# Optimization experiments

Hardware: AMD Instinct MI355X
Metric: run time of the kernel (lower is better)

## Reference

```python
import jax, jax.numpy as jnp
import numpy as np

SCALE = 16.0
IGNORE_THRES = 0.5
NUM_CLASSES = 40
ANCHORS_PX = np.array([[16., 16.], [32., 32.], [64., 64.], [32., 64.], [64., 32.]], dtype=np.float32)
NB, NA, NH, NW, MAXT = 16, 5, 96, 96, 50


def setup_inputs() -> dict:
    key = jax.random.key(0)
    k1, k2, k3, k4, k5, k6, k7 = jax.random.split(key, 7)
    prediction = jax.random.normal(k1, (NB, NA, NH, NW, 5 + NUM_CLASSES), jnp.float32)
    # GT boxes in pixel space; x in [0, NW*SCALE), y in [0, NH*SCALE)
    xs = jax.random.uniform(k2, (NB, MAXT), minval=0.5, maxval=NW - 0.5) * SCALE
    ys = jax.random.uniform(k3, (NB, MAXT), minval=0.5, maxval=NH - 0.5) * SCALE
    hs = jax.random.uniform(k4, (NB, MAXT), minval=0.5, maxval=6.0) * SCALE
    ws = jax.random.uniform(k5, (NB, MAXT), minval=0.5, maxval=6.0) * SCALE
    lbl = jax.random.randint(k6, (NB, MAXT), 0, NUM_CLASSES)
    target = jnp.zeros((NB, MAXT, 13 + NUM_CLASSES), jnp.float32)
    target = target.at[..., 0].set(xs).at[..., 1].set(ys)
    target = target.at[..., 3].set(hs).at[..., 4].set(ws)  # source reads h from col 3, w from col 4
    target = target.at[..., 13:].set(jax.nn.one_hot(lbl, NUM_CLASSES, dtype=jnp.float32))
    target_sizes = jax.random.randint(k7, (NB,), 20, MAXT + 1)
    return {"prediction": prediction, "target": target, "target_sizes": target_sizes}


def _iou_xywh(g, p):
    # center/size boxes -> corners, with the original's +1 pixel convention
    g_x1, g_x2 = g[0] - g[2] / 2, g[0] + g[2] / 2
    g_y1, g_y2 = g[1] - g[3] / 2, g[1] + g[3] / 2
    p_x1, p_x2 = p[0] - p[2] / 2, p[0] + p[2] / 2
    p_y1, p_y2 = p[1] - p[3] / 2, p[1] + p[3] / 2
    iw = jnp.clip(jnp.minimum(g_x2, p_x2) - jnp.maximum(g_x1, p_x1) + 1., 0.)
    ih = jnp.clip(jnp.minimum(g_y2, p_y2) - jnp.maximum(g_y1, p_y1) + 1., 0.)
    inter = iw * ih
    ga = (g_x2 - g_x1 + 1.) * (g_y2 - g_y1 + 1.)
    pa = (p_x2 - p_x1 + 1.) * (p_y2 - p_y1 + 1.)
    return inter / (ga + pa - inter + 1e-16)


def _build_targets(pred_boxes, pred_conf, pred_cls, target, target_sizes, anchors):
    # Sequential scan over (batch, gt) preserves the torch double-loop's
    nB, nA, nH, nW = pred_conf.shape
    maxT = target.shape[1]
    aw, ah = anchors[:, 0], anchors[:, 1]
    anch_area = (aw + 1.) * (ah + 1.)
    mask = jnp.zeros((nB, nA, nH, nW), jnp.float32)
    conf_mask = jnp.ones((nB, nA, nH, nW), jnp.float32)
    tx = jnp.zeros_like(mask); ty = jnp.zeros_like(mask)
    tw = jnp.zeros_like(mask); th = jnp.zeros_like(mask)
    tconf = jnp.zeros_like(mask)
    tlabel = jnp.zeros((nB, nA, nH, nW), jnp.int32)  # argmax of one-hot tcls

    def step(carry, bt):
        mask, conf_mask, tx, ty, tw, th, tconf, tlabel, nGT, nCorrect = carry
        b = bt // maxT
        t = bt % maxT
        valid = t < target_sizes[b]
        row = target[b, t]
        gx = row[0] / SCALE; gy = row[1] / SCALE
        gw = row[4] / SCALE; gh = row[3] / SCALE  # w from col 4, h from col 3 (as in source)
        gi = gx.astype(jnp.int32); gj = gy.astype(jnp.int32)
        # anchor IoU: both boxes anchored at origin, corner-style with +1 (x1y1x2y2=True path)
        inter = jnp.clip(jnp.minimum(gw, aw) + 1., 0.) * jnp.clip(jnp.minimum(gh, ah) + 1., 0.)
        anch_ious = inter / ((gw + 1.) * (gh + 1.) + anch_area - inter + 1e-16)
        bd = jnp.where(valid, b, nB)  # out-of-bounds batch index -> scatter dropped when padded
        cur = conf_mask[b, :, gj, gi]
        conf_mask = conf_mask.at[bd, :, gj, gi].set(jnp.where(anch_ious > IGNORE_THRES, 0., cur), mode='drop')
        best_n = jnp.argmax(anch_ious)
        mask = mask.at[bd, best_n, gj, gi].set(1., mode='drop')
        conf_mask = conf_mask.at[bd, best_n, gj, gi].set(1., mode='drop')
        tx = tx.at[bd, best_n, gj, gi].set(gx - gi.astype(jnp.float32), mode='drop')
        ty = ty.at[bd, best_n, gj, gi].set(gy - gj.astype(jnp.float32), mode='drop')
        tw = tw.at[bd, best_n, gj, gi].set(jnp.log(gw / aw[best_n] + 1e-16), mode='drop')
        th = th.at[bd, best_n, gj, gi].set(jnp.log(gh / ah[best_n] + 1e-16), mode='drop')
        lbl = jnp.argmax(row[13:]).astype(jnp.int32)
        tlabel = tlabel.at[bd, best_n, gj, gi].set(lbl, mode='drop')
        tconf = tconf.at[bd, best_n, gj, gi].set(1., mode='drop')
        iou = _iou_xywh(jnp.stack([gx, gy, gw, gh]), pred_boxes[b, best_n, gj, gi])
        correct = valid & (iou > 0.5) & (jnp.argmax(pred_cls[b, best_n, gj, gi]) == lbl) & (pred_conf[b, best_n, gj, gi] > 0.5)
        return (mask, conf_mask, tx, ty, tw, th, tconf, tlabel,
                nGT + valid.astype(jnp.int32), nCorrect + correct.astype(jnp.int32)), None

    init = (mask, conf_mask, tx, ty, tw, th, tconf, tlabel,
            jnp.array(0, jnp.int32), jnp.array(0, jnp.int32))
    (mask, conf_mask, tx, ty, tw, th, tconf, tlabel, nGT, nCorrect), _ = jax.lax.scan(
        step, init, jnp.arange(nB * maxT))
    return mask, conf_mask, tx, ty, tw, th, tconf, tlabel, nGT, nCorrect


def _yolo_loss(prediction, target, target_sizes):
    nB, nA, nH, nW = prediction.shape[:4]
    pred_conf = prediction[..., 0]
    x = prediction[..., 1]; y = prediction[..., 2]
    h = prediction[..., 3]; w = prediction[..., 4]
    pred_cls = prediction[..., 5:]
    grid_x = jnp.arange(nW, dtype=jnp.float32).reshape(1, 1, 1, nW)
    grid_y = jnp.arange(nH, dtype=jnp.float32).reshape(1, 1, nH, 1)
    anchors = jnp.asarray(ANCHORS_PX) / SCALE  # grid units
    aw = anchors[:, 0].reshape(1, nA, 1, 1)
    ah = anchors[:, 1].reshape(1, nA, 1, 1)
    pred_boxes = jnp.stack([
        x + grid_x, y + grid_y, jnp.exp(w) * aw * jnp.ones_like(w), jnp.exp(h) * ah * jnp.ones_like(h)
    ], axis=-1)
    sg = jax.lax.stop_gradient  # torch uses .cpu().data inside build_targets
    mask, conf_mask, tx, ty, tw, th, tconf, tlabel, nGT, nCorrect = _build_targets(
        sg(pred_boxes), sg(pred_conf), sg(pred_cls), target, target_sizes, anchors)
    nM = jnp.sum(mask)
    mmean = lambda v: jnp.sum(mask * v) / nM  # masked MSE mean (size_average=True)
    loss_x = mmean((x - tx) ** 2)
    loss_y = mmean((y - ty) ** 2)
    loss_w = mmean((w - tw) ** 2)
    loss_h = mmean((h - th) ** 2)
    # BCEWithLogits, numerically stable
    bce = jnp.maximum(pred_conf, 0.) - pred_conf * tconf + jnp.log1p(jnp.exp(-jnp.abs(pred_conf)))
    # torch: conf_mask_false = (conf_mask - mask) as byte used as boolean mask -> nonzero selects
    cmf = (conf_mask != mask).astype(jnp.float32)
    loss_conf = jnp.sum(cmf * bce) / jnp.sum(cmf) + jnp.sum(mask * bce) / nM
    logp = jax.nn.log_softmax(pred_cls, axis=-1)
    ce = -jnp.take_along_axis(logp, tlabel[..., None], axis=-1)[..., 0]
    loss_cls = (1.0 / nB) * jnp.sum(mask * ce) / nM
    loss = loss_x + loss_y + loss_w + loss_h + loss_conf + loss_cls
    nProposals = jnp.sum(pred_conf > 0).astype(jnp.float32)
    recall = nCorrect.astype(jnp.float32) / jnp.maximum(nGT, 1).astype(jnp.float32)
    precision = jnp.where(nProposals > 0, nCorrect.astype(jnp.float32) / jnp.maximum(nProposals, 1.), 1.0)
    return (loss, loss_x + loss_y + loss_w + loss_h, loss_conf, loss_cls, recall, precision)


def reference(prediction, target, target_sizes):
    return _yolo_loss(prediction, target, target_sizes)
```

## Files before the change

kernel.cpp:

```cpp
#include <hip/hip_runtime.h>
#include <math.h>

#define NB 16
#define NA 5
#define NH 96
#define NW 96
#define MAXT 50
#define NC 40
#define CH 45
#define TGT_W 53
#define NCELL (NH*NW)
#define NTGT (NB*MAXT)
#define TOTF4 8294400
#define CONF_BLOCKS 2025
#define CONF_STRIDE 2073600
#define IGNORE_THRES 0.5f

__device__ __constant__ float c_AW[5] = {1.f, 2.f, 4.f, 2.f, 4.f};
__device__ __constant__ float c_AH[5] = {1.f, 2.f, 4.f, 4.f, 2.f};


__device__ __forceinline__ float softplusf(float p) {
    return fmaxf(p, 0.f) + log1pf(expf(-fabsf(p)));
}

__device__ __forceinline__ float pick(float4 q, int comp) {
    return comp == 0 ? q.x : comp == 1 ? q.y : comp == 2 ? q.z : q.w;
}

__global__ __launch_bounds__(64) void tgt_phase1(
    const float* __restrict__ pred, const float* __restrict__ tgt,
    const int* __restrict__ tsz, double* acc, int* iacc,
    int* keyG, int* metaG, float* fxG, float* fyG, float* gwG, float* ghG) {
    const int bt = blockIdx.x;
    const int b = bt / MAXT, t = bt % MAXT;
    const int lane = threadIdx.x;

    if (bt == 0) {
        if (lane < 10) acc[lane] = 0.0;
        if (lane < 2)  iacc[lane] = 0;
    }

    const bool valid = t < tsz[b];
    const float* row = tgt + (size_t)bt * TGT_W;
    const float inv_s = 0.0625f;
    float gx = row[0] * inv_s, gy = row[1] * inv_s;
    float gh_ = row[3] * inv_s, gw_ = row[4] * inv_s;
    int gi = (int)gx, gj = (int)gy;

    float lv = (lane < NC) ? row[13 + lane] : -1e30f;
    int   li = (lane < NC) ? lane : (1 << 30);
    #pragma unroll
    for (int off = 32; off; off >>= 1) {
        float ov = __shfl_xor(lv, off);
        int   oi = __shfl_xor(li, off);
        if (ov > lv || (ov == lv && oi < li)) { lv = ov; li = oi; }
    }
    int lbl = li;

    float best_iou = -1e30f; int best = 0; int ign = 0;
    #pragma unroll
    for (int a = 0; a < 5; ++a) {
        float iw = fmaxf(fminf(gw_, c_AW[a]) + 1.f, 0.f);
        float ih = fmaxf(fminf(gh_, c_AH[a]) + 1.f, 0.f);
        float inter = iw * ih;
        float iou = inter / ((gw_ + 1.f) * (gh_ + 1.f) +
                             (c_AW[a] + 1.f) * (c_AH[a] + 1.f) - inter + 1e-16f);
        if (iou > IGNORE_THRES) ign |= (1 << a);
        if (iou > best_iou) { best_iou = iou; best = a; }
    }

    size_t pbase = ((((size_t)b * NA + best) * NH + gj) * NW + gi) * CH;
    float pv = (lane < CH) ? pred[pbase + lane] : -1e30f;
    float pc = __shfl(pv, 0);
    float px = __shfl(pv, 1) + (float)gi;
    float py = __shfl(pv, 2) + (float)gj;
    float ph = expf(__shfl(pv, 3)) * c_AH[best];
    float pw = expf(__shfl(pv, 4)) * c_AW[best];

    float gx1 = gx - gw_ * 0.5f, gx2 = gx + gw_ * 0.5f;
    float gy1 = gy - gh_ * 0.5f, gy2 = gy + gh_ * 0.5f;
    float px1 = px - pw * 0.5f, px2 = px + pw * 0.5f;
    float py1 = py - ph * 0.5f, py2 = py + ph * 0.5f;
    float iw2 = fmaxf(fminf(gx2, px2) - fmaxf(gx1, px1) + 1.f, 0.f);
    float ih2 = fmaxf(fminf(gy2, py2) - fmaxf(gy1, py1) + 1.f, 0.f);
    float inter2 = iw2 * ih2;
    float ga = (gx2 - gx1 + 1.f) * (gy2 - gy1 + 1.f);
    float pa = (px2 - px1 + 1.f) * (py2 - py1 + 1.f);
    float iou2 = inter2 / (ga + pa - inter2 + 1e-16f);

    float cv = (lane >= 5 && lane < CH) ? pv : -1e30f;
    int   ci = (lane >= 5 && lane < CH) ? (lane - 5) : (1 << 30);
    #pragma unroll
    for (int off = 32; off; off >>= 1) {
        float ov = __shfl_xor(cv, off);
        int   oi = __shfl_xor(ci, off);
        if (ov > cv || (ov == cv && oi < ci)) { cv = ov; ci = oi; }
    }
    bool correct = valid && (iou2 > 0.5f) && (ci == lbl) && (pc > 0.5f);

    if (lane == 0) {
        keyG[bt]  = valid ? (gj * NW + gi) : -1;
        metaG[bt] = best | (ign << 3) | (lbl << 8) | ((correct ? 1 : 0) << 14);
        fxG[bt] = gx - (float)gi; fyG[bt] = gy - (float)gj;
        gwG[bt] = gw_;            ghG[bt] = gh_;
    }
}

__global__ __launch_bounds__(64) void ownership(
    const int* __restrict__ keyG, const int* __restrict__ metaG,
    int* iacc, int* wlist) {
    __shared__ int sk[MAXT], sm[MAXT];
    const int b = blockIdx.x, t = threadIdx.x;
    if (t < MAXT) { sk[t] = keyG[b * MAXT + t]; sm[t] = metaG[b * MAXT + t]; }
    __syncthreads();
    if (t >= MAXT) return;
    const int myKey = sk[t];
    if (myKey < 0) return;
    for (int u = t + 1; u < MAXT; ++u)
        if (sk[u] == myKey) return;

    int cm = 0x1F, m = 0;
    int w[5] = {-1, -1, -1, -1, -1};
    for (int u = 0; u < MAXT; ++u) {
        if (sk[u] != myKey) continue;
        int mu = sm[u];
        cm &= ~((mu >> 3) & 0x1F);
        int bn = mu & 7;
        cm |= (1 << bn); m |= (1 << bn);
        w[bn] = u;
    }
    int pos = atomicAdd(&iacc[1], 5);
    #pragma unroll
    for (int a = 0; a < 5; ++a) {
        int ca = (b * NA + a) * NCELL + myKey;
        int flags = ca | (((m >> a) & 1) << 20) | (((cm >> a) & 1) << 21);
        wlist[2 * (pos + a)]     = flags;
        wlist[2 * (pos + a) + 1] = ((m >> a) & 1) ? (b * MAXT + w[a]) : -1;
    }
}

__global__ __launch_bounds__(1024) void corrections(
    const float* __restrict__ pred, double* acc, const int* __restrict__ iacc,
    const int* __restrict__ wlist, const int* __restrict__ metaG,
    const float* __restrict__ fxG, const float* __restrict__ fyG,
    const float* __restrict__ gwG, const float* __restrict__ ghG) {
    const int wave = threadIdx.x >> 6, lane = threadIdx.x & 63;
    const int idx = blockIdx.x * 16 + wave;
    const int count = iacc[1];
    double loc[9];
    #pragma unroll
    for (int c = 0; c < 9; ++c) loc[c] = 0.0;

    if (idx < count) {
        int flags = wlist[2 * idx], writer = wlist[2 * idx + 1];
        int ca = flags & 0xFFFFF;
        int ma = (flags >> 20) & 1, cma = (flags >> 21) & 1;
        size_t base = (size_t)ca * CH;
        float v = (lane < CH) ? pred[base + lane] : -1e30f;
        float p = __shfl(v, 0);
        float s0 = softplusf(p);
        int cmf = (cma != ma) ? 1 : 0;
        loc[0] = (cmf ? (double)(s0 - p * (float)ma) : 0.0) - (double)s0;
        loc[1] = (double)(cmf - 1);
        if (ma) {
            loc[2] = (double)(s0 - p);
            loc[8] = 1.0;
            float x = __shfl(v, 1), y = __shfl(v, 2);
            float hh = __shfl(v, 3), wv = __shfl(v, 4);
            float fx = fxG[writer], fy = fyG[writer];
            float gww = gwG[writer], ghh = ghG[writer];
            int a = (ca / NCELL) % NA;
            int lbl = (metaG[writer] >> 8) & 0x3F;
            float tw_ = logf(gww / c_AW[a] + 1e-16f);
            float th_ = logf(ghh / c_AH[a] + 1e-16f);
            loc[4] = (double)((x - fx) * (x - fx));
            loc[5] = (double)((y - fy) * (y - fy));
            loc[6] = (double)((wv - tw_) * (wv - tw_));
            loc[7] = (double)((hh - th_) * (hh - th_));
            float cvv = (lane >= 5 && lane < CH) ? v : -1e30f;
            float mx = cvv;
            #pragma unroll
            for (int off = 32; off; off >>= 1) mx = fmaxf(mx, __shfl_xor(mx, off));
            float e = (lane >= 5 && lane < CH) ? expf(v - mx) : 0.f;
            #pragma unroll
            for (int off = 32; off; off >>= 1) e += __shfl_xor(e, off);
            float cll = __shfl(v, 5 + lbl);
            loc[3] = (double)(logf(e) + mx - cll);
        }
    }

    __shared__ double red[16][9];
    if (lane == 0) {
        #pragma unroll
        for (int c = 0; c < 9; ++c) red[wave][c] = loc[c];
    }
    __syncthreads();
    if (threadIdx.x < 9) {
        double s = 0.0;
        #pragma unroll
        for (int wv = 0; wv < 16; ++wv) s += red[wv][threadIdx.x];
        if (s != 0.0) atomicAdd(&acc[1 + threadIdx.x], s);
    }
}

__global__ __launch_bounds__(1024) void conf_pass3(
    const float4* __restrict__ pf, double* partial_d, int* partial_i) {
    const int tid = blockIdx.x * 1024 + threadIdx.x;
    float4 q0 = pf[tid];
    float4 q1 = pf[tid + CONF_STRIDE];
    float4 q2 = pf[tid + 2 * CONF_STRIDE];
    float4 q3 = pf[tid + 3 * CONF_STRIDE];

    float bce = 0.f; int prop = 0;
    int r = tid % 45;
    if (r == 0 || r == 11 || r == 22 || r == 33) {
        int comp = r / 11;
        float c0 = pick(q0, comp), c1 = pick(q1, comp);
        float c2 = pick(q2, comp), c3 = pick(q3, comp);
        bce = softplusf(c0) + softplusf(c1) + softplusf(c2) + softplusf(c3);
        prop = (c0 > 0.f) + (c1 > 0.f) + (c2 > 0.f) + (c3 > 0.f);
    }

    #pragma unroll
    for (int off = 32; off; off >>= 1) {
        bce  += __shfl_down(bce, off);
        prop += __shfl_down(prop, off);
    }
    __shared__ float sb[16];
    __shared__ int   sp[16];
    int wid = threadIdx.x >> 6, lane = threadIdx.x & 63;
    if (lane == 0) { sb[wid] = bce; sp[wid] = prop; }
    __syncthreads();
    if (threadIdx.x == 0) {
        float tb = 0.f; int tp = 0;
        #pragma unroll
        for (int w = 0; w < 16; ++w) { tb += sb[w]; tp += sp[w]; }
        partial_d[blockIdx.x] = (double)tb;
        partial_i[blockIdx.x] = tp;
    }
}

__global__ __launch_bounds__(256) void finalize(
    const double* __restrict__ acc, const int* __restrict__ iacc,
    const int* __restrict__ tsz, const int* __restrict__ metaG,
    const double* __restrict__ partial_d, const int* __restrict__ partial_i,
    float* out) {
    __shared__ double sd[256];
    __shared__ int    si[256], sc[256];
    double db = 0.0; int ip = 0, cor = 0;
    for (int i = threadIdx.x; i < CONF_BLOCKS; i += 256) { db += partial_d[i]; ip += partial_i[i]; }
    for (int i = threadIdx.x; i < NTGT; i += 256) cor += (metaG[i] >> 14) & 1;
    sd[threadIdx.x] = db; si[threadIdx.x] = ip; sc[threadIdx.x] = cor;
    __syncthreads();
    for (int off = 128; off; off >>= 1) {
        if (threadIdx.x < off) {
            sd[threadIdx.x] += sd[threadIdx.x + off];
            si[threadIdx.x] += si[threadIdx.x + off];
            sc[threadIdx.x] += sc[threadIdx.x + off];
        }
        __syncthreads();
    }
    if (threadIdx.x != 0) return;
    double sum_bce0 = sd[0];
    int nProp = si[0], nCor = sc[0];
    int nGT = 0;
    for (int b = 0; b < NB; ++b) nGT += tsz[b];

    double nM = acc[9];
    double inv_nM = 1.0 / (nM > 0.0 ? nM : 1e-16);
    double l_coord = (acc[5] + acc[6] + acc[7] + acc[8]) * inv_nM;
    double sum_cmf = (double)(NB * NA * NH * NW) + acc[2];
    double l_conf = (sum_bce0 + acc[1]) / sum_cmf + acc[3] * inv_nM;
    double l_cls = (1.0 / (double)NB) * acc[4] * inv_nM;
    double loss = l_coord + l_conf + l_cls;
    float recall = (float)nCor / (float)(nGT > 1 ? nGT : 1);
    float precision = (nProp > 0) ? ((float)nCor / fmaxf((float)nProp, 1.f)) : 1.f;
    out[0] = (float)loss;
    out[1] = (float)l_coord;
    out[2] = (float)l_conf;
    out[3] = (float)l_cls;
    out[4] = recall;
    out[5] = precision;
}

extern "C" void kernel_launch(void* const* d_in, const int* in_sizes, int n_in,
                              void* d_out, int out_size, void* d_ws, size_t ws_size,
                              hipStream_t stream) {
    const float* pred = (const float*)d_in[0];
    const float* tgt  = (const float*)d_in[1];
    const int*   tsz  = (const int*)d_in[2];
    float* out = (float*)d_out;

    double* acc = (double*)d_ws;
    int* iacc   = (int*)((char*)d_ws + 80);
    int* keyG   = (int*)((char*)d_ws + 96);
    int* metaG  = keyG + NTGT;
    float* fxG  = (float*)(metaG + NTGT);
    float* fyG  = fxG + NTGT;
    float* gwG  = fyG + NTGT;
    float* ghG  = gwG + NTGT;
    int* wlist  = (int*)(ghG + NTGT);
    double* partial_d = (double*)((char*)d_ws + 51296);
    int*    partial_i = (int*)((char*)d_ws + 67496);

    tgt_phase1<<<NTGT, 64, 0, stream>>>(pred, tgt, tsz, acc, iacc,
                                        keyG, metaG, fxG, fyG, gwG, ghG);
    ownership<<<NB, 64, 0, stream>>>(keyG, metaG, iacc, wlist);
    corrections<<<250, 1024, 0, stream>>>(pred, acc, iacc, wlist,
                                          metaG, fxG, fyG, gwG, ghG);
    conf_pass3<<<CONF_BLOCKS, 1024, 0, stream>>>((const float4*)pred, partial_d, partial_i);
    finalize<<<1, 256, 0, stream>>>(acc, iacc, tsz, metaG, partial_d, partial_i, out);
}
```

Baseline: 217.9 us.

## Fuse target building with ownership and merge corrections into the conf pass

Merges the per-target and ownership kernels into a single per-batch kernel that uses shared memory. It writes fixed slots containing precomputed targets, which removes the atomic slot counter. The corrections pass and the full confidence reduction now run in one launch, partitioned by block index, and each conf thread reads 8 float4s instead of 4. The goal is to cut launch count and serial dependencies. The cost is fewer, heavier conf blocks, and the per-batch target kernel runs on only 16 blocks.

```diff
diff --git a/kernel.cpp b/kernel.cpp
--- a/kernel.cpp
+++ b/kernel.cpp
@@ -12,8 +12,10 @@
 #define NCELL (NH*NW)
 #define NTGT (NB*MAXT)
 #define TOTF4 8294400
-#define CONF_BLOCKS 2025
-#define CONF_STRIDE 2073600
+#define S8 1036800
+#define CONF_BLOCKS 1013
+#define CORR_BLOCKS 250
+#define NSLOT 4000
 #define IGNORE_THRES 0.5f
 
 __device__ __constant__ float c_AW[5] = {1.f, 2.f, 4.f, 2.f, 4.f};
@@ -28,244 +30,265 @@
     return comp == 0 ? q.x : comp == 1 ? q.y : comp == 2 ? q.z : q.w;
 }
 
-__global__ __launch_bounds__(64) void tgt_phase1(
+__global__ __launch_bounds__(1024) void tgt_build(
     const float* __restrict__ pred, const float* __restrict__ tgt,
-    const int* __restrict__ tsz, double* acc, int* iacc,
-    int* keyG, int* metaG, float* fxG, float* fyG, float* gwG, float* ghG) {
-    const int bt = blockIdx.x;
-    const int b = bt / MAXT, t = bt % MAXT;
-    const int lane = threadIdx.x;
-
-    if (bt == 0) {
-        if (lane < 10) acc[lane] = 0.0;
-        if (lane < 2)  iacc[lane] = 0;
-    }
-
-    const bool valid = t < tsz[b];
-    const float* row = tgt + (size_t)bt * TGT_W;
-    const float inv_s = 0.0625f;
-    float gx = row[0] * inv_s, gy = row[1] * inv_s;
-    float gh_ = row[3] * inv_s, gw_ = row[4] * inv_s;
-    int gi = (int)gx, gj = (int)gy;
-
-    float lv = (lane < NC) ? row[13 + lane] : -1e30f;
-    int   li = (lane < NC) ? lane : (1 << 30);
-    #pragma unroll
-    for (int off = 32; off; off >>= 1) {
-        float ov = __shfl_xor(lv, off);
-        int   oi = __shfl_xor(li, off);
-        if (ov > lv || (ov == lv && oi < li)) { lv = ov; li = oi; }
-    }
-    int lbl = li;
-
-    float best_iou = -1e30f; int best = 0; int ign = 0;
-    #pragma unroll
-    for (int a = 0; a < 5; ++a) {
-        float iw = fmaxf(fminf(gw_, c_AW[a]) + 1.f, 0.f);
-        float ih = fmaxf(fminf(gh_, c_AH[a]) + 1.f, 0.f);
-        float inter = iw * ih;
-        float iou = inter / ((gw_ + 1.f) * (gh_ + 1.f) +
-                             (c_AW[a] + 1.f) * (c_AH[a] + 1.f) - inter + 1e-16f);
-        if (iou > IGNORE_THRES) ign |= (1 << a);
-        if (iou > best_iou) { best_iou = iou; best = a; }
-    }
-
-    size_t pbase = ((((size_t)b * NA + best) * NH + gj) * NW + gi) * CH;
-    float pv = (lane < CH) ? pred[pbase + lane] : -1e30f;
-    float pc = __shfl(pv, 0);
-    float px = __shfl(pv, 1) + (float)gi;
-    float py = __shfl(pv, 2) + (float)gj;
-    float ph = expf(__shfl(pv, 3)) * c_AH[best];
-    float pw = expf(__shfl(pv, 4)) * c_AW[best];
-
-    float gx1 = gx - gw_ * 0.5f, gx2 = gx + gw_ * 0.5f;
-    float gy1 = gy - gh_ * 0.5f, gy2 = gy + gh_ * 0.5f;
-    float px1 = px - pw * 0.5f, px2 = px + pw * 0.5f;
-    float py1 = py - ph * 0.5f, py2 = py + ph * 0.5f;
-    float iw2 = fmaxf(fminf(gx2, px2) - fmaxf(gx1, px1) + 1.f, 0.f);
-    float ih2 = fmaxf(fminf(gy2, py2) - fmaxf(gy1, py1) + 1.f, 0.f);
-    float inter2 = iw2 * ih2;
-    float ga = (gx2 - gx1 + 1.f) * (gy2 - gy1 + 1.f);
-    float pa = (px2 - px1 + 1.f) * (py2 - py1 + 1.f);
-    float iou2 = inter2 / (ga + pa - inter2 + 1e-16f);
-
-    float cv = (lane >= 5 && lane < CH) ? pv : -1e30f;
-    int   ci = (lane >= 5 && lane < CH) ? (lane - 5) : (1 << 30);
-    #pragma unroll
-    for (int off = 32; off; off >>= 1) {
-        float ov = __shfl_xor(cv, off);
-        int   oi = __shfl_xor(ci, off);
-        if (ov > cv || (ov == cv && oi < ci)) { cv = ov; ci = oi; }
-    }
-    bool correct = valid && (iou2 > 0.5f) && (ci == lbl) && (pc > 0.5f);
-
-    if (lane == 0) {
-        keyG[bt]  = valid ? (gj * NW + gi) : -1;
-        metaG[bt] = best | (ign << 3) | (lbl << 8) | ((correct ? 1 : 0) << 14);
-        fxG[bt] = gx - (float)gi; fyG[bt] = gy - (float)gj;
-        gwG[bt] = gw_;            ghG[bt] = gh_;
-    }
-}
-
-__global__ __launch_bounds__(64) void ownership(
-    const int* __restrict__ keyG, const int* __restrict__ metaG,
-    int* iacc, int* wlist) {
-    __shared__ int sk[MAXT], sm[MAXT];
-    const int b = blockIdx.x, t = threadIdx.x;
-    if (t < MAXT) { sk[t] = keyG[b * MAXT + t]; sm[t] = metaG[b * MAXT + t]; }
+    const int* __restrict__ tsz, double* acc, int* corG, int* wlist) {
+    __shared__ int   s_key[MAXT], s_best[MAXT], s_ign[MAXT], s_lbl[MAXT];
+    __shared__ float s_fx[MAXT], s_fy[MAXT], s_gw[MAXT], s_gh[MAXT];
+    __shared__ int   s_cor[MAXT];
+
+    const int b = blockIdx.x;
+    const int wave = threadIdx.x >> 6, lane = threadIdx.x & 63;
+
+    if (b == 0 && threadIdx.x < 10) acc[threadIdx.x] = 0.0;
+
+    const int size_b = tsz[b];
+
+    for (int t = wave; t < MAXT; t += 16) {
+        const bool valid = t < size_b;
+        const float* row = tgt + ((size_t)b * MAXT + t) * TGT_W;
+        const float inv_s = 0.0625f;
+        float gx = row[0] * inv_s, gy = row[1] * inv_s;
+        float gh_ = row[3] * inv_s, gw_ = row[4] * inv_s;
+        int gi = (int)gx, gj = (int)gy;
+
+        float lv = (lane < NC) ? row[13 + lane] : -1e30f;
+        int   li = (lane < NC) ? lane : (1 << 30);
+        #pragma unroll
+        for (int off = 32; off; off >>= 1) {
+            float ov = __shfl_xor(lv, off);
+            int   oi = __shfl_xor(li, off);
+            if (ov > lv || (ov == lv && oi < li)) { lv = ov; li = oi; }
+        }
+        int lbl = li;
+
+        float best_iou = -1e30f; int best = 0; int ign = 0;
+        #pragma unroll
+        for (int a = 0; a < 5; ++a) {
+            float iw = fmaxf(fminf(gw_, c_AW[a]) + 1.f, 0.f);
+            float ih = fmaxf(fminf(gh_, c_AH[a]) + 1.f, 0.f);
+            float inter = iw * ih;
+            float iou = inter / ((gw_ + 1.f) * (gh_ + 1.f) +
+                                 (c_AW[a] + 1.f) * (c_AH[a] + 1.f) - inter + 1e-16f);
+            if (iou > IGNORE_THRES) ign |= (1 << a);
+            if (iou > best_iou) { best_iou = iou; best = a; }
+        }
+
+        size_t pbase = ((((size_t)b * NA + best) * NH + gj) * NW + gi) * CH;
+        float pv = (lane < CH) ? pred[pbase + lane] : -1e30f;
+        float pc = __shfl(pv, 0);
+        float px = __shfl(pv, 1) + (float)gi;
+        float py = __shfl(pv, 2) + (float)gj;
+        float ph = expf(__shfl(pv, 3)) * c_AH[best];
+        float pw = expf(__shfl(pv, 4)) * c_AW[best];
+
+        float gx1 = gx - gw_ * 0.5f, gx2 = gx + gw_ * 0.5f;
+        float gy1 = gy - gh_ * 0.5f, gy2 = gy + gh_ * 0.5f;
+        float px1 = px - pw * 0.5f, px2 = px + pw * 0.5f;
+        float py1 = py - ph * 0.5f, py2 = py + ph * 0.5f;
+        float iw2 = fmaxf(fminf(gx2, px2) - fmaxf(gx1, px1) + 1.f, 0.f);
+        float ih2 = fmaxf(fminf(gy2, py2) - fmaxf(gy1, py1) + 1.f, 0.f);
+        float inter2 = iw2 * ih2;
+        float ga = (gx2 - gx1 + 1.f) * (gy2 - gy1 + 1.f);
+        float pa = (px2 - px1 + 1.f) * (py2 - py1 + 1.f);
+        float iou2 = inter2 / (ga + pa - inter2 + 1e-16f);
+
+        float cv = (lane >= 5 && lane < CH) ? pv : -1e30f;
+        int   ci = (lane >= 5 && lane < CH) ? (lane - 5) : (1 << 30);
+        #pragma unroll
+        for (int off = 32; off; off >>= 1) {
+            float ov = __shfl_xor(cv, off);
+            int   oi = __shfl_xor(ci, off);
+            if (ov > cv || (ov == cv && oi < ci)) { cv = ov; ci = oi; }
+        }
+        bool correct = valid && (iou2 > 0.5f) && (ci == lbl) && (pc > 0.5f);
+
+        if (lane == 0) {
+            s_key[t] = valid ? (gj * NW + gi) : -1;
+            s_best[t] = best; s_ign[t] = ign; s_lbl[t] = lbl;
+            s_fx[t] = gx - (float)gi; s_fy[t] = gy - (float)gj;
+            s_gw[t] = gw_; s_gh[t] = gh_;
+            s_cor[t] = correct ? 1 : 0;
+        }
+    }
     __syncthreads();
+
+    if (threadIdx.x == 0) {
+        int c = 0;
+        for (int t = 0; t < MAXT; ++t) c += s_cor[t];
+        corG[b] = c;
+    }
+
+    const int t = threadIdx.x;
     if (t >= MAXT) return;
-    const int myKey = sk[t];
-    if (myKey < 0) return;
-    for (int u = t + 1; u < MAXT; ++u)
-        if (sk[u] == myKey) return;
+    int* slot0 = wlist + ((size_t)(b * MAXT + t) * NA) * 8;
+
+    const int myKey = s_key[t];
+    bool owner = (myKey >= 0);
+    if (owner)
+        for (int u = t + 1; u < MAXT; ++u)
+            if (s_key[u] == myKey) { owner = false; break; }
+
+    if (!owner) {
+        #pragma unroll
+        for (int a = 0; a < 5; ++a) slot0[a * 8] = 0;
+        return;
+    }
 
     int cm = 0x1F, m = 0;
     int w[5] = {-1, -1, -1, -1, -1};
     for (int u = 0; u < MAXT; ++u) {
-        if (sk[u] != myKey) continue;
-        int mu = sm[u];
-        cm &= ~((mu >> 3) & 0x1F);
-        int bn = mu & 7;
+        if (s_key[u] != myKey) continue;
+        cm &= ~s_ign[u];
+        int bn = s_best[u];
         cm |= (1 << bn); m |= (1 << bn);
         w[bn] = u;
     }
-    int pos = atomicAdd(&iacc[1], 5);
     #pragma unroll
     for (int a = 0; a < 5; ++a) {
+        int* e = slot0 + a * 8;
         int ca = (b * NA + a) * NCELL + myKey;
-        int flags = ca | (((m >> a) & 1) << 20) | (((cm >> a) & 1) << 21);
-        wlist[2 * (pos + a)]     = flags;
-        wlist[2 * (pos + a) + 1] = ((m >> a) & 1) ? (b * MAXT + w[a]) : -1;
-    }
-}
-
-__global__ __launch_bounds__(1024) void corrections(
-    const float* __restrict__ pred, double* acc, const int* __restrict__ iacc,
-    const int* __restrict__ wlist, const int* __restrict__ metaG,
-    const float* __restrict__ fxG, const float* __restrict__ fyG,
-    const float* __restrict__ gwG, const float* __restrict__ ghG) {
+        int ma = (m >> a) & 1, cma = (cm >> a) & 1;
+        e[0] = ca | (ma << 20) | (cma << 21) | (1 << 22);
+        if (ma) {
+            int u = w[a];
+            e[1] = s_lbl[u];
+            e[2] = __float_as_int(s_fx[u]);
+            e[3] = __float_as_int(s_fy[u]);
+            e[4] = __float_as_int(logf(s_gw[u] / c_AW[a] + 1e-16f));
+            e[5] = __float_as_int(logf(s_gh[u] / c_AH[a] + 1e-16f));
+        }
+    }
+}
+
+__global__ __launch_bounds__(1024) void mega(
+    const float* __restrict__ pred, double* acc, const int* __restrict__ wlist,
+    double* partial_d, int* partial_i) {
     const int wave = threadIdx.x >> 6, lane = threadIdx.x & 63;
-    const int idx = blockIdx.x * 16 + wave;
-    const int count = iacc[1];
-    double loc[9];
-    #pragma unroll
-    for (int c = 0; c < 9; ++c) loc[c] = 0.0;
-
-    if (idx < count) {
-        int flags = wlist[2 * idx], writer = wlist[2 * idx + 1];
-        int ca = flags & 0xFFFFF;
-        int ma = (flags >> 20) & 1, cma = (flags >> 21) & 1;
-        size_t base = (size_t)ca * CH;
-        float v = (lane < CH) ? pred[base + lane] : -1e30f;
-        float p = __shfl(v, 0);
-        float s0 = softplusf(p);
-        int cmf = (cma != ma) ? 1 : 0;
-        loc[0] = (cmf ? (double)(s0 - p * (float)ma) : 0.0) - (double)s0;
-        loc[1] = (double)(cmf - 1);
-        if (ma) {
-            loc[2] = (double)(s0 - p);
-            loc[8] = 1.0;
-            float x = __shfl(v, 1), y = __shfl(v, 2);
-            float hh = __shfl(v, 3), wv = __shfl(v, 4);
-            float fx = fxG[writer], fy = fyG[writer];
-            float gww = gwG[writer], ghh = ghG[writer];
-            int a = (ca / NCELL) % NA;
-            int lbl = (metaG[writer] >> 8) & 0x3F;
-            float tw_ = logf(gww / c_AW[a] + 1e-16f);
-            float th_ = logf(ghh / c_AH[a] + 1e-16f);
-            loc[4] = (double)((x - fx) * (x - fx));
-            loc[5] = (double)((y - fy) * (y - fy));
-            loc[6] = (double)((wv - tw_) * (wv - tw_));
-            loc[7] = (double)((hh - th_) * (hh - th_));
-            float cvv = (lane >= 5 && lane < CH) ? v : -1e30f;
-            float mx = cvv;
+
+    if (blockIdx.x < CORR_BLOCKS) {
+        const int s = blockIdx.x * 16 + wave;
+        const int* e = wlist + (size_t)s * 8;
+        double loc[9];
+        #pragma unroll
+        for (int c = 0; c < 9; ++c) loc[c] = 0.0;
+
+        int flags = e[0];
+        if (flags & (1 << 22)) {
+            int ca = flags & 0xFFFFF;
+            int ma = (flags >> 20) & 1, cma = (flags >> 21) & 1;
+            size_t base = (size_t)ca * CH;
+            float v = (lane < CH) ? pred[base + lane] : -1e30f;
+            float p = __shfl(v, 0);
+            float s0 = softplusf(p);
+            int cmf = (cma != ma) ? 1 : 0;
+            loc[0] = (cmf ? (double)(s0 - p * (float)ma) : 0.0) - (double)s0;
+            loc[1] = (double)(cmf - 1);
+            if (ma) {
+                loc[2] = (double)(s0 - p);
+                loc[8] = 1.0;
+                float x = __shfl(v, 1), y = __shfl(v, 2);
+                float hh = __shfl(v, 3), wv = __shfl(v, 4);
+                float fx = __int_as_float(e[2]), fy = __int_as_float(e[3]);
+                float tw_ = __int_as_float(e[4]), th_ = __int_as_float(e[5]);
+                int lbl = e[1];
+                loc[4] = (double)((x - fx) * (x - fx));
+                loc[5] = (double)((y - fy) * (y - fy));
+                loc[6] = (double)((wv - tw_) * (wv - tw_));
+                loc[7] = (double)((hh - th_) * (hh - th_));
+                float cvv = (lane >= 5 && lane < CH) ? v : -1e30f;
+                float mx = cvv;
+                #pragma unroll
+                for (int off = 32; off; off >>= 1) mx = fmaxf(mx, __shfl_xor(mx, off));
+                float ex = (lane >= 5 && lane < CH) ? expf(v - mx) : 0.f;
+                #pragma unroll
+                for (int off = 32; off; off >>= 1) ex += __shfl_xor(ex, off);
+                float cll = __shfl(v, 5 + lbl);
+                loc[3] = (double)(logf(ex) + mx - cll);
+            }
+        }
+
+        __shared__ double red[16][9];
+        if (lane == 0) {
             #pragma unroll
-            for (int off = 32; off; off >>= 1) mx = fmaxf(mx, __shfl_xor(mx, off));
-            float e = (lane >= 5 && lane < CH) ? expf(v - mx) : 0.f;
+            for (int c = 0; c < 9; ++c) red[wave][c] = loc[c];
+        }
+        __syncthreads();
+        if (threadIdx.x < 9) {
+            double sum = 0.0;
             #pragma unroll
-            for (int off = 32; off; off >>= 1) e += __shfl_xor(e, off);
-            float cll = __shfl(v, 5 + lbl);
-            loc[3] = (double)(logf(e) + mx - cll);
-        }
-    }
-
-    __shared__ double red[16][9];
-    if (lane == 0) {
-        #pragma unroll
-        for (int c = 0; c < 9; ++c) red[wave][c] = loc[c];
-    }
-    __syncthreads();
-    if (threadIdx.x < 9) {
-        double s = 0.0;
-        #pragma unroll
-        for (int wv = 0; wv < 16; ++wv) s += red[wv][threadIdx.x];
-        if (s != 0.0) atomicAdd(&acc[1 + threadIdx.x], s);
-    }
-}
-
-__global__ __launch_bounds__(1024) void conf_pass3(
-    const float4* __restrict__ pf, double* partial_d, int* partial_i) {
-    const int tid = blockIdx.x * 1024 + threadIdx.x;
-    float4 q0 = pf[tid];
-    float4 q1 = pf[tid + CONF_STRIDE];
-    float4 q2 = pf[tid + 2 * CONF_STRIDE];
-    float4 q3 = pf[tid + 3 * CONF_STRIDE];
-
-    float bce = 0.f; int prop = 0;
-    int r = tid % 45;
-    if (r == 0 || r == 11 || r == 22 || r == 33) {
-        int comp = r / 11;
-        float c0 = pick(q0, comp), c1 = pick(q1, comp);
-        float c2 = pick(q2, comp), c3 = pick(q3, comp);
-        bce = softplusf(c0) + softplusf(c1) + softplusf(c2) + softplusf(c3);
-        prop = (c0 > 0.f) + (c1 > 0.f) + (c2 > 0.f) + (c3 > 0.f);
-    }
-
-    #pragma unroll
-    for (int off = 32; off; off >>= 1) {
-        bce  += __shfl_down(bce, off);
-        prop += __shfl_down(prop, off);
-    }
-    __shared__ float sb[16];
-    __shared__ int   sp[16];
-    int wid = threadIdx.x >> 6, lane = threadIdx.x & 63;
-    if (lane == 0) { sb[wid] = bce; sp[wid] = prop; }
-    __syncthreads();
-    if (threadIdx.x == 0) {
-        float tb = 0.f; int tp = 0;
-        #pragma unroll
-        for (int w = 0; w < 16; ++w) { tb += sb[w]; tp += sp[w]; }
-        partial_d[blockIdx.x] = (double)tb;
-        partial_i[blockIdx.x] = tp;
+            for (int wv = 0; wv < 16; ++wv) sum += red[wv][threadIdx.x];
+            if (sum != 0.0) atomicAdd(&acc[1 + threadIdx.x], sum);
+        }
+    } else {
+        const int cb = blockIdx.x - CORR_BLOCKS;
+        const int tid = cb * 1024 + threadIdx.x;
+        const float4* pf = (const float4*)pred;
+        float bce = 0.f; int prop = 0;
+        if (tid < S8) {
+            float4 q0 = pf[tid];
+            float4 q1 = pf[tid + S8];
+            float4 q2 = pf[tid + 2 * S8];
+            float4 q3 = pf[tid + 3 * S8];
+            float4 q4 = pf[tid + 4 * S8];
+            float4 q5 = pf[tid + 5 * S8];
+            float4 q6 = pf[tid + 6 * S8];
+            float4 q7 = pf[tid + 7 * S8];
+            int r = tid % 45;
+            if (r == 0 || r == 11 || r == 22 || r == 33) {
+                int comp = r / 11;
+                float c0 = pick(q0, comp), c1 = pick(q1, comp);
+                float c2 = pick(q2, comp), c3 = pick(q3, comp);
+                float c4 = pick(q4, comp), c5 = pick(q5, comp);
+                float c6 = pick(q6, comp), c7 = pick(q7, comp);
+                bce = softplusf(c0) + softplusf(c1) + softplusf(c2) + softplusf(c3)
+                    + softplusf(c4) + softplusf(c5) + softplusf(c6) + softplusf(c7);
+                prop = (c0 > 0.f) + (c1 > 0.f) + (c2 > 0.f) + (c3 > 0.f)
+                     + (c4 > 0.f) + (c5 > 0.f) + (c6 > 0.f) + (c7 > 0.f);
+            }
+        }
+        #pragma unroll
+        for (int off = 32; off; off >>= 1) {
+            bce  += __shfl_down(bce, off);
+            prop += __shfl_down(prop, off);
+        }
+        __shared__ float sb[16];
+        __shared__ int   sp[16];
+        if (lane == 0) { sb[wave] = bce; sp[wave] = prop; }
+        __syncthreads();
+        if (threadIdx.x == 0) {
+            float tb = 0.f; int tp = 0;
+            #pragma unroll
+            for (int wv = 0; wv < 16; ++wv) { tb += sb[wv]; tp += sp[wv]; }
+            partial_d[cb] = (double)tb;
+            partial_i[cb] = tp;
+        }
     }
 }
 
 __global__ __launch_bounds__(256) void finalize(
-    const double* __restrict__ acc, const int* __restrict__ iacc,
-    const int* __restrict__ tsz, const int* __restrict__ metaG,
+    const double* __restrict__ acc, const int* __restrict__ corG,
+    const int* __restrict__ tsz,
     const double* __restrict__ partial_d, const int* __restrict__ partial_i,
     float* out) {
     __shared__ double sd[256];
-    __shared__ int    si[256], sc[256];
-    double db = 0.0; int ip = 0, cor = 0;
+    __shared__ int    si[256];
+    double db = 0.0; int ip = 0;
     for (int i = threadIdx.x; i < CONF_BLOCKS; i += 256) { db += partial_d[i]; ip += partial_i[i]; }
-    for (int i = threadIdx.x; i < NTGT; i += 256) cor += (metaG[i] >> 14) & 1;
-    sd[threadIdx.x] = db; si[threadIdx.x] = ip; sc[threadIdx.x] = cor;
+    sd[threadIdx.x] = db; si[threadIdx.x] = ip;
     __syncthreads();
     for (int off = 128; off; off >>= 1) {
         if (threadIdx.x < off) {
             sd[threadIdx.x] += sd[threadIdx.x + off];
             si[threadIdx.x] += si[threadIdx.x + off];
-            sc[threadIdx.x] += sc[threadIdx.x + off];
         }
         __syncthreads();
     }
     if (threadIdx.x != 0) return;
     double sum_bce0 = sd[0];
-    int nProp = si[0], nCor = sc[0];
-    int nGT = 0;
-    for (int b = 0; b < NB; ++b) nGT += tsz[b];
+    int nProp = si[0];
+    int nCor = 0, nGT = 0;
+    for (int b = 0; b < NB; ++b) { nCor += corG[b]; nGT += tsz[b]; }
 
     double nM = acc[9];
     double inv_nM = 1.0 / (nM > 0.0 ? nM : 1e-16);
@@ -293,22 +316,13 @@
     float* out = (float*)d_out;
 
     double* acc = (double*)d_ws;
-    int* iacc   = (int*)((char*)d_ws + 80);
-    int* keyG   = (int*)((char*)d_ws + 96);
-    int* metaG  = keyG + NTGT;
-    float* fxG  = (float*)(metaG + NTGT);
-    float* fyG  = fxG + NTGT;
-    float* gwG  = fyG + NTGT;
-    float* ghG  = gwG + NTGT;
-    int* wlist  = (int*)(ghG + NTGT);
-    double* partial_d = (double*)((char*)d_ws + 51296);
-    int*    partial_i = (int*)((char*)d_ws + 67496);
-
-    tgt_phase1<<<NTGT, 64, 0, stream>>>(pred, tgt, tsz, acc, iacc,
-                                        keyG, metaG, fxG, fyG, gwG, ghG);
-    ownership<<<NB, 64, 0, stream>>>(keyG, metaG, iacc, wlist);
-    corrections<<<250, 1024, 0, stream>>>(pred, acc, iacc, wlist,
-                                          metaG, fxG, fyG, gwG, ghG);
-    conf_pass3<<<CONF_BLOCKS, 1024, 0, stream>>>((const float4*)pred, partial_d, partial_i);
-    finalize<<<1, 256, 0, stream>>>(acc, iacc, tsz, metaG, partial_d, partial_i, out);
-}
+    int* corG   = (int*)((char*)d_ws + 80);
+    int* wlist  = (int*)((char*)d_ws + 160);
+    double* partial_d = (double*)((char*)d_ws + 512160);
+    int*    partial_i = (int*)((char*)d_ws + 520264);
+
+    tgt_build<<<NB, 1024, 0, stream>>>(pred, tgt, tsz, acc, corG, wlist);
+    mega<<<CORR_BLOCKS + CONF_BLOCKS, 1024, 0, stream>>>(pred, acc, wlist,
+                                                         partial_d, partial_i);
+    finalize<<<1, 256, 0, stream>>>(acc, corG, tsz, partial_d, partial_i, out);
+}
```

Result: no change. 221.1 us (+1.5%).
